# Kernel optimization log

Measured on AMD Instinct MI355X. Metric: run time of the kernel, lower is better.

Reference implementation:

```python
import jax, jax.numpy as jnp
import numpy as np

N_NODES = 400000
N_EDGES = 800000
DIM = 128
N_LAYER = 5
ATOM_VOCAB = 119   # len(possible_atomic_num_list)
CHIR_VOCAB = 4     # len(possible_chirality_list)
BN_EPS = 1e-5


def setup_inputs() -> dict:
    key = jax.random.key(0)
    ks = jax.random.split(key, 12)
    x = jax.random.randint(ks[0], (N_NODES, 2), 0, 4, dtype=jnp.int64 if jax.config.read('jax_enable_x64') else jnp.int32).astype(jnp.int32)
    edge_index = jax.random.randint(ks[1], (2, N_EDGES), 0, N_NODES).astype(jnp.int32)
    edge_attr = jax.random.randint(ks[2], (N_EDGES, 1), 0, 4).astype(jnp.int32)
    s = 0.02
    emb_atom = jax.random.normal(ks[3], (ATOM_VOCAB, DIM), jnp.float32) * s
    emb_chir = jax.random.normal(ks[4], (CHIR_VOCAB, DIM), jnp.float32) * s
    W1 = jax.random.normal(ks[5], (N_LAYER, DIM, DIM), jnp.float32) * s
    b1 = jnp.zeros((N_LAYER, DIM), jnp.float32)
    W2 = jax.random.normal(ks[6], (N_LAYER, DIM, DIM), jnp.float32) * s
    b2 = jnp.zeros((N_LAYER, DIM), jnp.float32)
    gamma = jnp.ones((N_LAYER, DIM), jnp.float32)
    beta = jnp.zeros((N_LAYER, DIM), jnp.float32)
    return {"x": x, "edge_index": edge_index, "edge_attr": edge_attr,
            "emb_atom": emb_atom, "emb_chir": emb_chir,
            "W1": W1, "b1": b1, "W2": W2, "b2": b2,
            "gamma": gamma, "beta": beta}


def _batch_norm_train(z, g, b):
    # BatchNorm1d in training mode: batch statistics over node axis
    mean = jnp.mean(z, axis=0)
    var = jnp.mean(jnp.square(z - mean), axis=0)  # biased var, as torch BN
    return (z - mean) * jax.lax.rsqrt(var + BN_EPS) * g + b


def reference(x, edge_index, edge_attr, emb_atom, emb_chir, W1, b1, W2, b2, gamma, beta):
    # summed per-column node embeddings (drop_ratio=0 -> dropout is identity)
    h = emb_atom[x[:, 0]] + emb_chir[x[:, 1]]           # [N, D]
    src, dst = edge_index[0], edge_index[1]
    n = h.shape[0]
    L = W1.shape[0]
    for l in range(L):
        # GINConv, eps=0: mlp((1+eps)*h_i + sum_{j->i} h_j)
        agg = jax.ops.segment_sum(h[src], dst, num_segments=n)  # gather-scatter
        z = h + agg
        z = jax.nn.relu(z @ W1[l] + b1[l]) @ W2[l] + b2[l]       # MLP([D, D, D])
        z = _batch_norm_train(z, gamma[l], beta[l])
        if l < L - 1:
            z = jax.nn.relu(z)
        h = z
    return h
```

## Files before the change

### kernel.cpp

```cpp
#include <hip/hip_runtime.h>
#include <hip/hip_bf16.h>

#define N_NODES 400000
#define N_EDGES 800000
#define DIM 128
#define NLAYER 5
#define BN_EPS 1e-5f

typedef _Float16 half8 __attribute__((ext_vector_type(8)));
typedef _Float16 half4 __attribute__((ext_vector_type(4)));
typedef _Float16 half2v __attribute__((ext_vector_type(2)));
typedef float f32x4 __attribute__((ext_vector_type(4)));

__global__ __launch_bounds__(256) void k_embed(const int* __restrict__ x,
                                               const float* __restrict__ ea,
                                               const float* __restrict__ ec,
                                               _Float16* __restrict__ out) {
  int idx = blockIdx.x * 256 + threadIdx.x;
  int i = idx >> 4, c8 = (idx & 15) * 8;
  int av = x[2 * i], cv = x[2 * i + 1];
  float4 a0 = *(const float4*)(ea + (size_t)av * DIM + c8);
  float4 a1 = *(const float4*)(ea + (size_t)av * DIM + c8 + 4);
  float4 c0 = *(const float4*)(ec + (size_t)cv * DIM + c8);
  float4 c1 = *(const float4*)(ec + (size_t)cv * DIM + c8 + 4);
  half8 r;
  r[0] = (_Float16)(a0.x + c0.x); r[1] = (_Float16)(a0.y + c0.y);
  r[2] = (_Float16)(a0.z + c0.z); r[3] = (_Float16)(a0.w + c0.w);
  r[4] = (_Float16)(a1.x + c1.x); r[5] = (_Float16)(a1.y + c1.y);
  r[6] = (_Float16)(a1.z + c1.z); r[7] = (_Float16)(a1.w + c1.w);
  *(half8*)(out + (size_t)i * DIM + c8) = r;
}

__global__ __launch_bounds__(256) void k_hist(const int* __restrict__ dst, int* __restrict__ cnt) {
  int e = blockIdx.x * 256 + threadIdx.x;
  if (e < N_EDGES) atomicAdd(&cnt[dst[e]], 1);
}

__global__ __launch_bounds__(256) void k_scan1(const int* __restrict__ cnt, int* __restrict__ rp,
                                               int* __restrict__ part) {
  __shared__ int sm[256];
  int t = threadIdx.x;
  int base = blockIdx.x * 1024 + t * 4;
  int v0 = 0, v1 = 0, v2 = 0, v3 = 0;
  if (base + 4 <= N_NODES) {
    int4 v = *(const int4*)(cnt + base);
    v0 = v.x; v1 = v.y; v2 = v.z; v3 = v.w;
  } else {
    if (base     < N_NODES) v0 = cnt[base];
    if (base + 1 < N_NODES) v1 = cnt[base + 1];
    if (base + 2 < N_NODES) v2 = cnt[base + 2];
    if (base + 3 < N_NODES) v3 = cnt[base + 3];
  }
  int s = v0 + v1 + v2 + v3;
  sm[t] = s;
  __syncthreads();
  for (int off = 1; off < 256; off <<= 1) {
    int add = (t >= off) ? sm[t - off] : 0;
    __syncthreads();
    sm[t] += add;
    __syncthreads();
  }
  int incl = sm[t];
  int ex = incl - s;
  if (t == 255) part[blockIdx.x] = incl;
  if (base     < N_NODES) rp[base]     = ex;
  if (base + 1 < N_NODES) rp[base + 1] = ex + v0;
  if (base + 2 < N_NODES) rp[base + 2] = ex + v0 + v1;
  if (base + 3 < N_NODES) rp[base + 3] = ex + v0 + v1 + v2;
}

__global__ __launch_bounds__(512) void k_scan2(int* __restrict__ part, int nb) {
  __shared__ int sm[512];
  int t = threadIdx.x;
  int v = (t < nb) ? part[t] : 0;
  sm[t] = v;
  __syncthreads();
  for (int off = 1; off < 512; off <<= 1) {
    int add = (t >= off) ? sm[t - off] : 0;
    __syncthreads();
    sm[t] += add;
    __syncthreads();
  }
  if (t < nb) part[t] = sm[t] - v;
}

__global__ __launch_bounds__(256) void k_scan3(int* __restrict__ rp, const int* __restrict__ part) {
  int i = blockIdx.x * 256 + threadIdx.x;
  if (i < N_NODES) rp[i] += part[i >> 10];
  if (i == 0) rp[N_NODES] = N_EDGES;
}

__global__ __launch_bounds__(256) void k_scatter(const int* __restrict__ src, const int* __restrict__ dst,
                                                 const int* __restrict__ rp, int* __restrict__ fill,
                                                 int* __restrict__ es) {
  int e = blockIdx.x * 256 + threadIdx.x;
  if (e < N_EDGES) {
    int d = dst[e];
    int slot = rp[d] + atomicAdd(&fill[d], 1);
    es[slot] = src[e];
  }
}

__global__ __launch_bounds__(128) void k_wprep(const float* __restrict__ W1, const float* __restrict__ W2,
                                               _Float16* __restrict__ wt) {
  int b = blockIdx.x;
  int l = b >> 8, mat = (b >> 7) & 1, c = b & 127;
  int k = threadIdx.x;
  const float* W = mat ? W2 : W1;
  float v = W[(size_t)l * DIM * DIM + (size_t)k * DIM + c];
  wt[((size_t)(l * 2 + mat) * DIM + c) * DIM + k] = (_Float16)v;
}

template <int UA>
__global__ __launch_bounds__(256) void k_aggx(const _Float16* __restrict__ P, const int* __restrict__ rp,
                                              const int* __restrict__ es, const float* __restrict__ affine,
                                              _Float16* __restrict__ X) {
  const int lane = threadIdx.x & 63;
  const int g = lane >> 4, gl = lane & 15;
  const int wid = (blockIdx.x * 256 + threadIdx.x) >> 6;
  const int nid = wid * 4 + g;
  const int c8 = gl * 8;

  float a[8], c[8];
  if (UA) {
    float4 t0 = *(const float4*)(affine + c8);
    float4 t1 = *(const float4*)(affine + c8 + 4);
    float4 u0 = *(const float4*)(affine + DIM + c8);
    float4 u1 = *(const float4*)(affine + DIM + c8 + 4);
    a[0] = t0.x; a[1] = t0.y; a[2] = t0.z; a[3] = t0.w;
    a[4] = t1.x; a[5] = t1.y; a[6] = t1.z; a[7] = t1.w;
    c[0] = u0.x; c[1] = u0.y; c[2] = u0.z; c[3] = u0.w;
    c[4] = u1.x; c[5] = u1.y; c[6] = u1.z; c[7] = u1.w;
  }
  const int e0 = rp[nid], e1 = rp[nid + 1];

  half8 sv = *(const half8*)(P + (size_t)nid * DIM + c8);
  float sx[8], tx[8];
#pragma unroll
  for (int i = 0; i < 8; ++i) {
    float v = (float)sv[i];
    sx[i] = UA ? fmaxf(fmaf(a[i], v, c[i]), 0.f) : v;
    tx[i] = 0.f;
  }
  for (int base = e0; base < e1; base += 16) {
    int n = e1 - base; if (n > 16) n = 16;
    int esr = (base + gl < e1) ? es[base + gl] : 0;
    int j = 0;
    for (; j + 2 <= n; j += 2) {
      int s0 = __shfl(esr, (g << 4) + j);
      int s1 = __shfl(esr, (g << 4) + j + 1);
      half8 v0 = *(const half8*)(P + (size_t)s0 * DIM + c8);
      half8 v1 = *(const half8*)(P + (size_t)s1 * DIM + c8);
#pragma unroll
      for (int i = 0; i < 8; ++i) {
        float f0 = (float)v0[i], f1 = (float)v1[i];
        if (UA) {
          f0 = fmaxf(fmaf(a[i], f0, c[i]), 0.f);
          f1 = fmaxf(fmaf(a[i], f1, c[i]), 0.f);
        }
        sx[i] += f0; tx[i] += f1;
      }
    }
    if (j < n) {
      int s0 = __shfl(esr, (g << 4) + j);
      half8 v0 = *(const half8*)(P + (size_t)s0 * DIM + c8);
#pragma unroll
      for (int i = 0; i < 8; ++i) {
        float f0 = (float)v0[i];
        if (UA) f0 = fmaxf(fmaf(a[i], f0, c[i]), 0.f);
        sx[i] += f0;
      }
    }
  }
  half8 r;
#pragma unroll
  for (int i = 0; i < 8; ++i) r[i] = (_Float16)(sx[i] + tx[i]);
  *(half8*)(X + (size_t)nid * DIM + c8) = r;
}

__global__ __launch_bounds__(256) void k_mlp(const _Float16* __restrict__ X,
                                             const _Float16* __restrict__ wt,
                                             const float* __restrict__ b1, const float* __restrict__ b2,
                                             _Float16* __restrict__ Z, float* __restrict__ stats) {
  __shared__ _Float16 sh[16384 * 2 + 64 * DIM];
  _Float16* w1t = sh;
  _Float16* w2t = sh + 16384;
  _Float16* tb  = sh + 32768;

  const int tid = threadIdx.x;
  const int lane = tid & 63, w = tid >> 6;
  const int l15 = lane & 15, h = lane >> 4;

  const half8* wg = (const half8*)wt;
#pragma unroll
  for (int i = 0; i < 16; ++i) {
    int h8 = i * 256 + tid;
    half8 v = wg[h8];
    int idx8 = h8 & 2047;
    int c = idx8 >> 4, k8 = idx8 & 15;
    int hidx = (h8 >> 11) * 16384 + c * DIM + k8 * 8;
    hidx ^= ((c & 7) << 3);
    *(half8*)(sh + hidx) = v;
  }

  const int row = blockIdx.x * 64 + 16 * w + l15;
  const size_t rbase = (size_t)row * DIM;
  half8 xf[4];
#pragma unroll
  for (int kt = 0; kt < 4; ++kt)
    xf[kt] = *(const half8*)(X + rbase + kt * 32 + 8 * h);
  __syncthreads();

#pragma unroll
  for (int ct = 0; ct < 8; ++ct) {
    int n = ct * 16 + l15;
    float bv = b1[n];
    f32x4 acc = {bv, bv, bv, bv};
#pragma unroll
    for (int kt = 0; kt < 4; ++kt) {
      int hidx = n * DIM + kt * 32 + 8 * h;
      hidx ^= ((n & 7) << 3);
      half8 bf = *(const half8*)(w1t + hidx);
      acc = __builtin_amdgcn_mfma_f32_16x16x32_f16(xf[kt], bf, acc, 0, 0, 0);
    }
#pragma unroll
    for (int r = 0; r < 4; ++r) {
      int lr = 16 * w + 4 * h + r;
      int ti = lr * DIM + n;
      ti ^= ((lr & 7) << 3);
      tb[ti] = (_Float16)fmaxf(acc[r], 0.f);
    }
  }
  __syncthreads();

  half8 tf[4];
#pragma unroll
  for (int kt = 0; kt < 4; ++kt) {
    int lr = 16 * w + l15;
    int ti = lr * DIM + kt * 32 + 8 * h;
    ti ^= ((lr & 7) << 3);
    tf[kt] = *(const half8*)(tb + ti);
  }
  float* sst = (float*)sh;
  sst[tid] = 0.f;
  __syncthreads();

  float sa[8], qa[8];
#pragma unroll
  for (int ct = 0; ct < 8; ++ct) {
    int n = ct * 16 + l15;
    float bv = b2[n];
    f32x4 acc = {bv, bv, bv, bv};
#pragma unroll
    for (int kt = 0; kt < 4; ++kt) {
      int hidx = n * DIM + kt * 32 + 8 * h;
      hidx ^= ((n & 7) << 3);
      half8 bf = *(const half8*)(w2t + hidx);
      acc = __builtin_amdgcn_mfma_f32_16x16x32_f16(tf[kt], bf, acc, 0, 0, 0);
    }
    float s = 0.f, q = 0.f;
#pragma unroll
    for (int r = 0; r < 4; ++r) {
      int lr = 16 * w + 4 * h + r;
      float y = acc[r];
      int ti = lr * DIM + n;
      ti ^= ((lr & 7) << 3);
      tb[ti] = (_Float16)y;
      s += y; q += y * y;
    }
    sa[ct] = s; qa[ct] = q;
  }
#pragma unroll
  for (int ct = 0; ct < 8; ++ct) {
    float s = sa[ct], q = qa[ct];
    s += __shfl_xor(s, 16); s += __shfl_xor(s, 32);
    q += __shfl_xor(q, 16); q += __shfl_xor(q, 32);
    if (h == 0) {
      int n = ct * 16 + l15;
      atomicAdd(&sst[n], s);
      atomicAdd(&sst[DIM + n], q);
    }
  }
  __syncthreads();

#pragma unroll
  for (int i = 0; i < 4; ++i) {
    int chunk = i * 256 + tid;
    int lr = chunk >> 4, k8 = chunk & 15;
    int ti = (lr * DIM + k8 * 8) ^ ((lr & 7) << 3);
    half8 v = *(const half8*)(tb + ti);
    *(half8*)(Z + (size_t)(blockIdx.x * 64 + lr) * DIM + k8 * 8) = v;
  }
  atomicAdd(&stats[(blockIdx.x & 63) * 256 + tid], sst[tid]);
}

__global__ __launch_bounds__(128) void k_fin(const float* __restrict__ stats, const float* __restrict__ gamma,
                                             const float* __restrict__ beta, float* __restrict__ affine) {
  int c = threadIdx.x;
  float s = 0.f, q = 0.f;
  for (int i = 0; i < 64; ++i) {
    s += stats[i * 256 + c];
    q += stats[i * 256 + DIM + c];
  }
  float mean = s / (float)N_NODES;
  float var = q / (float)N_NODES - mean * mean;
  float inv = 1.f / sqrtf(var + BN_EPS);
  float a = gamma[c] * inv;
  affine[c] = a;
  affine[DIM + c] = beta[c] - mean * a;
}

__global__ __launch_bounds__(256) void k_out(const _Float16* __restrict__ z, const float* __restrict__ affine,
                                             float* __restrict__ out) {
  int idx = blockIdx.x * 256 + threadIdx.x;
  int c4 = (idx & 31) * 4;
  half4 v = *(const half4*)(z + (size_t)idx * 4);
  float4 a = *(const float4*)(affine + c4);
  float4 c = *(const float4*)(affine + DIM + c4);
  float4 r;
  r.x = fmaf(a.x, (float)v[0], c.x); r.y = fmaf(a.y, (float)v[1], c.y);
  r.z = fmaf(a.z, (float)v[2], c.z); r.w = fmaf(a.w, (float)v[3], c.w);
  *(float4*)(out + (size_t)idx * 4) = r;
}

extern "C" void kernel_launch(void* const* d_in, const int* in_sizes, int n_in,
                              void* d_out, int out_size, void* d_ws, size_t ws_size,
                              hipStream_t stream) {
  const int*   x     = (const int*)d_in[0];
  const int*   ei    = (const int*)d_in[1];
  const float* ea    = (const float*)d_in[3];
  const float* ec    = (const float*)d_in[4];
  const float* W1    = (const float*)d_in[5];
  const float* b1    = (const float*)d_in[6];
  const float* W2    = (const float*)d_in[7];
  const float* b2    = (const float*)d_in[8];
  const float* gamma = (const float*)d_in[9];
  const float* beta  = (const float*)d_in[10];
  const int* src = ei;
  const int* dst = ei + N_EDGES;

  char* ws = (char*)d_ws;
  size_t off = 0;
  auto take = [&](size_t b) { char* p = ws + off; off += (b + 255) & ~(size_t)255; return p; };
  _Float16* Z0     = (_Float16*)take((size_t)N_NODES * DIM * 2);
  _Float16* Z1     = (_Float16*)take((size_t)N_NODES * DIM * 2);
  _Float16* X      = (_Float16*)take((size_t)N_NODES * DIM * 2);
  _Float16* wt     = (_Float16*)take((size_t)NLAYER * 2 * DIM * DIM * 2);
  int*      rp     = (int*)take((size_t)(N_NODES + 1) * 4);
  int*      fill   = (int*)take((size_t)N_NODES * 4);
  int*      es     = (int*)take((size_t)N_EDGES * 4);
  int*      part   = (int*)take(4096);
  float*    stats  = (float*)take(64 * 256 * 4);
  float*    affine = (float*)take(256 * 4);
  if (off > ws_size) return;

  const int NB1 = (N_NODES + 1023) / 1024;

  hipMemsetAsync(fill, 0, (size_t)N_NODES * 4, stream);
  k_hist<<<(N_EDGES + 255) / 256, 256, 0, stream>>>(dst, fill);
  k_scan1<<<NB1, 256, 0, stream>>>(fill, rp, part);
  k_scan2<<<1, 512, 0, stream>>>(part, NB1);
  k_scan3<<<(N_NODES + 255) / 256, 256, 0, stream>>>(rp, part);
  hipMemsetAsync(fill, 0, (size_t)N_NODES * 4, stream);
  k_scatter<<<(N_EDGES + 255) / 256, 256, 0, stream>>>(src, dst, rp, fill, es);

  k_embed<<<N_NODES * 16 / 256, 256, 0, stream>>>(x, ea, ec, Z0);
  k_wprep<<<NLAYER * 2 * DIM, DIM, 0, stream>>>(W1, W2, wt);

  _Float16* pin = Z0;
  _Float16* pout = Z1;
  for (int l = 0; l < NLAYER; ++l) {
    if (l == 0)
      k_aggx<0><<<N_NODES / 16, 256, 0, stream>>>(pin, rp, es, affine, X);
    else
      k_aggx<1><<<N_NODES / 16, 256, 0, stream>>>(pin, rp, es, affine, X);
    hipMemsetAsync(stats, 0, 64 * 256 * 4, stream);
    k_mlp<<<N_NODES / 64, 256, 0, stream>>>(X, wt + (size_t)l * 2 * DIM * DIM,
                                            b1 + l * DIM, b2 + l * DIM, pout, stats);
    k_fin<<<1, DIM, 0, stream>>>(stats, gamma + l * DIM, beta + l * DIM, affine);
    _Float16* t = pin; pin = pout; pout = t;
  }
  k_out<<<N_NODES * 32 / 256, 256, 0, stream>>>(pin, affine, (float*)d_out);
}
```

Before: 1.250 ms.

## Halve MLP shared memory by reusing one weight buffer and unroll gather by four

The MLP kernel now keeps a single 32KB weight buffer: W1 is loaded first, then W2 overwrites it after the first GEMM. Total LDS per block drops from 80KB to 48KB, so more blocks can be resident per CU. The cost is serialising the W2 load behind the first GEMM, plus an extra barrier. The aggregation kernel also unrolls the neighbour gather to four loads per iteration, using zero weights to mask the tail, which raises memory-level parallelism at the cost of some wasted loads.

```diff
diff --git a/kernel.cpp b/kernel.cpp
--- a/kernel.cpp
+++ b/kernel.cpp
@@ -9,7 +9,6 @@
 
 typedef _Float16 half8 __attribute__((ext_vector_type(8)));
 typedef _Float16 half4 __attribute__((ext_vector_type(4)));
-typedef _Float16 half2v __attribute__((ext_vector_type(2)));
 typedef float f32x4 __attribute__((ext_vector_type(4)));
 
 __global__ __launch_bounds__(256) void k_embed(const int* __restrict__ x,
@@ -135,46 +134,44 @@
   const int e0 = rp[nid], e1 = rp[nid + 1];
 
   half8 sv = *(const half8*)(P + (size_t)nid * DIM + c8);
-  float sx[8], tx[8];
+  float sx[8];
 #pragma unroll
   for (int i = 0; i < 8; ++i) {
     float v = (float)sv[i];
     sx[i] = UA ? fmaxf(fmaf(a[i], v, c[i]), 0.f) : v;
-    tx[i] = 0.f;
   }
   for (int base = e0; base < e1; base += 16) {
     int n = e1 - base; if (n > 16) n = 16;
     int esr = (base + gl < e1) ? es[base + gl] : 0;
-    int j = 0;
-    for (; j + 2 <= n; j += 2) {
+    for (int j = 0; j < n; j += 4) {
       int s0 = __shfl(esr, (g << 4) + j);
       int s1 = __shfl(esr, (g << 4) + j + 1);
+      int s2 = __shfl(esr, (g << 4) + j + 2);
+      int s3 = __shfl(esr, (g << 4) + j + 3);
+      float w1 = (j + 1 < n) ? 1.f : 0.f;
+      float w2 = (j + 2 < n) ? 1.f : 0.f;
+      float w3 = (j + 3 < n) ? 1.f : 0.f;
       half8 v0 = *(const half8*)(P + (size_t)s0 * DIM + c8);
       half8 v1 = *(const half8*)(P + (size_t)s1 * DIM + c8);
+      half8 v2 = *(const half8*)(P + (size_t)s2 * DIM + c8);
+      half8 v3 = *(const half8*)(P + (size_t)s3 * DIM + c8);
 #pragma unroll
       for (int i = 0; i < 8; ++i) {
         float f0 = (float)v0[i], f1 = (float)v1[i];
+        float f2 = (float)v2[i], f3 = (float)v3[i];
         if (UA) {
           f0 = fmaxf(fmaf(a[i], f0, c[i]), 0.f);
           f1 = fmaxf(fmaf(a[i], f1, c[i]), 0.f);
+          f2 = fmaxf(fmaf(a[i], f2, c[i]), 0.f);
+          f3 = fmaxf(fmaf(a[i], f3, c[i]), 0.f);
         }
-        sx[i] += f0; tx[i] += f1;
+        sx[i] += f0 + w1 * f1 + w2 * f2 + w3 * f3;
       }
     }
-    if (j < n) {
-      int s0 = __shfl(esr, (g << 4) + j);
-      half8 v0 = *(const half8*)(P + (size_t)s0 * DIM + c8);
-#pragma unroll
-      for (int i = 0; i < 8; ++i) {
-        float f0 = (float)v0[i];
-        if (UA) f0 = fmaxf(fmaf(a[i], f0, c[i]), 0.f);
-        sx[i] += f0;
-      }
-    }
   }
   half8 r;
 #pragma unroll
-  for (int i = 0; i < 8; ++i) r[i] = (_Float16)(sx[i] + tx[i]);
+  for (int i = 0; i < 8; ++i) r[i] = (_Float16)sx[i];
   *(half8*)(X + (size_t)nid * DIM + c8) = r;
 }
 
@@ -182,25 +179,22 @@
                                              const _Float16* __restrict__ wt,
                                              const float* __restrict__ b1, const float* __restrict__ b2,
                                              _Float16* __restrict__ Z, float* __restrict__ stats) {
-  __shared__ _Float16 sh[16384 * 2 + 64 * DIM];
-  _Float16* w1t = sh;
-  _Float16* w2t = sh + 16384;
-  _Float16* tb  = sh + 32768;
+  __shared__ _Float16 sh[16384 + 64 * DIM];
+  _Float16* wbuf = sh;
+  _Float16* tb   = sh + 16384;
 
   const int tid = threadIdx.x;
   const int lane = tid & 63, w = tid >> 6;
   const int l15 = lane & 15, h = lane >> 4;
-
   const half8* wg = (const half8*)wt;
-#pragma unroll
-  for (int i = 0; i < 16; ++i) {
+
+#pragma unroll
+  for (int i = 0; i < 8; ++i) {
     int h8 = i * 256 + tid;
     half8 v = wg[h8];
-    int idx8 = h8 & 2047;
-    int c = idx8 >> 4, k8 = idx8 & 15;
-    int hidx = (h8 >> 11) * 16384 + c * DIM + k8 * 8;
-    hidx ^= ((c & 7) << 3);
-    *(half8*)(sh + hidx) = v;
+    int cc = h8 >> 4, k8 = h8 & 15;
+    int hidx = (cc * DIM + k8 * 8) ^ ((cc & 7) << 3);
+    *(half8*)(wbuf + hidx) = v;
   }
 
   const int row = blockIdx.x * 64 + 16 * w + l15;
@@ -218,31 +212,35 @@
     f32x4 acc = {bv, bv, bv, bv};
 #pragma unroll
     for (int kt = 0; kt < 4; ++kt) {
-      int hidx = n * DIM + kt * 32 + 8 * h;
-      hidx ^= ((n & 7) << 3);
-      half8 bf = *(const half8*)(w1t + hidx);
+      int hidx = (n * DIM + kt * 32 + 8 * h) ^ ((n & 7) << 3);
+      half8 bf = *(const half8*)(wbuf + hidx);
       acc = __builtin_amdgcn_mfma_f32_16x16x32_f16(xf[kt], bf, acc, 0, 0, 0);
     }
 #pragma unroll
     for (int r = 0; r < 4; ++r) {
       int lr = 16 * w + 4 * h + r;
-      int ti = lr * DIM + n;
-      ti ^= ((lr & 7) << 3);
+      int ti = (lr * DIM + n) ^ ((lr & 7) << 3);
       tb[ti] = (_Float16)fmaxf(acc[r], 0.f);
     }
   }
   __syncthreads();
 
+#pragma unroll
+  for (int i = 0; i < 8; ++i) {
+    int h8 = 2048 + i * 256 + tid;
+    half8 v = wg[h8];
+    int idx8 = h8 & 2047;
+    int cc = idx8 >> 4, k8 = idx8 & 15;
+    int hidx = (cc * DIM + k8 * 8) ^ ((cc & 7) << 3);
+    *(half8*)(wbuf + hidx) = v;
+  }
   half8 tf[4];
 #pragma unroll
   for (int kt = 0; kt < 4; ++kt) {
     int lr = 16 * w + l15;
-    int ti = lr * DIM + kt * 32 + 8 * h;
-    ti ^= ((lr & 7) << 3);
+    int ti = (lr * DIM + kt * 32 + 8 * h) ^ ((lr & 7) << 3);
     tf[kt] = *(const half8*)(tb + ti);
   }
-  float* sst = (float*)sh;
-  sst[tid] = 0.f;
   __syncthreads();
 
   float sa[8], qa[8];
@@ -253,9 +251,8 @@
     f32x4 acc = {bv, bv, bv, bv};
 #pragma unroll
     for (int kt = 0; kt < 4; ++kt) {
-      int hidx = n * DIM + kt * 32 + 8 * h;
-      hidx ^= ((n & 7) << 3);
-      half8 bf = *(const half8*)(w2t + hidx);
+      int hidx = (n * DIM + kt * 32 + 8 * h) ^ ((n & 7) << 3);
+      half8 bf = *(const half8*)(wbuf + hidx);
       acc = __builtin_amdgcn_mfma_f32_16x16x32_f16(tf[kt], bf, acc, 0, 0, 0);
     }
     float s = 0.f, q = 0.f;
@@ -263,13 +260,17 @@
     for (int r = 0; r < 4; ++r) {
       int lr = 16 * w + 4 * h + r;
       float y = acc[r];
-      int ti = lr * DIM + n;
-      ti ^= ((lr & 7) << 3);
+      int ti = (lr * DIM + n) ^ ((lr & 7) << 3);
       tb[ti] = (_Float16)y;
       s += y; q += y * y;
     }
     sa[ct] = s; qa[ct] = q;
   }
+  __syncthreads();
+
+  float* sst = (float*)sh;
+  sst[tid] = 0.f;
+  __syncthreads();
 #pragma unroll
   for (int ct = 0; ct < 8; ++ct) {
     float s = sa[ct], q = qa[ct];
```

After: 1.189 ms. -4.9%, faster.
